# Optimization experiments

Hardware: AMD Instinct MI355X
Metric: run time of the kernel (lower is better)

Reference implementation:

```python
import jax, jax.numpy as jnp
import numpy as np

B, S, H = 1, 1024, 2048
NH, NKV, HD = 32, 4, 128
E, K, I = 32, 8, 768
EPS = 1e-06
ROPE_BASE = 1e6


def rmsnorm(x, w, eps=EPS):
    xf = x.astype(jnp.float32)
    var = jnp.mean(xf * xf, axis=-1, keepdims=True)
    return w * (xf * jax.lax.rsqrt(var + eps)).astype(x.dtype)


def apply_rope(x, cos, sin):
    # x: [B,S,N,HD]; cos/sin: [S,HD//2]; interleaved (llama-style) pair rotation
    xr = x.reshape(*x.shape[:-1], HD // 2, 2)
    x0, x1 = xr[..., 0], xr[..., 1]
    c = cos[None, :, None, :]
    s = sin[None, :, None, :]
    o0 = x0 * c - x1 * s
    o1 = x0 * s + x1 * c
    return jnp.stack([o0, o1], axis=-1).reshape(x.shape)


def setup_inputs() -> dict:
    key = jax.random.key(0)
    ks = jax.random.split(key, 16)
    hidden_states = jax.random.normal(ks[0], (B, S, H), dtype=jnp.float32)
    # RoPE angles: positions * inv_freq  -> [S, HD//2]
    inv_freq = 1.0 / (ROPE_BASE ** (np.arange(0, HD, 2, dtype=np.float32) / HD))
    position_embeddings = jnp.asarray(np.arange(S, dtype=np.float32)[:, None] * inv_freq[None, :])
    # causal additive mask [1,1,S,S]
    causal = jnp.tril(jnp.ones((S, S), dtype=bool))
    attention_mask = jnp.where(causal, 0.0, -1e9).astype(jnp.float32)[None, None]
    w = 0.02
    params = {
        'ln1_w': jnp.ones((H,), jnp.float32),
        'ln2_w': jnp.ones((H,), jnp.float32),
        'q_w': w * jax.random.normal(ks[1], (H, NH * HD), jnp.float32),
        'k_w': w * jax.random.normal(ks[2], (H, NKV * HD), jnp.float32),
        'v_w': w * jax.random.normal(ks[3], (H, NKV * HD), jnp.float32),
        'o_w': w * jax.random.normal(ks[4], (NH * HD, H), jnp.float32),
        'qn_w': jnp.ones((HD,), jnp.float32),
        'kn_w': jnp.ones((HD,), jnp.float32),
        'gate_w': w * jax.random.normal(ks[5], (H, E), jnp.float32),
        'wg': w * jax.random.normal(ks[6], (E, H, I), jnp.float32),
        'wu': w * jax.random.normal(ks[7], (E, H, I), jnp.float32),
        'wd': w * jax.random.normal(ks[8], (E, I, H), jnp.float32),
    }
    return {'hidden_states': hidden_states, 'position_embeddings': position_embeddings,
            'attention_mask': attention_mask, 'start_pos': 0, **params}


def reference(hidden_states, position_embeddings, attention_mask, start_pos,
              ln1_w, ln2_w, q_w, k_w, v_w, o_w, qn_w, kn_w, gate_w, wg, wu, wd):
    x = hidden_states  # [B,S,H]
    # --- attention ---
    h = rmsnorm(x, ln1_w)
    q = rmsnorm((h @ q_w).reshape(B, S, NH, HD), qn_w)
    k = rmsnorm((h @ k_w).reshape(B, S, NKV, HD), kn_w)
    v = (h @ v_w).reshape(B, S, NKV, HD)
    cos, sin = jnp.cos(position_embeddings), jnp.sin(position_embeddings)
    q = apply_rope(q, cos, sin)
    k = apply_rope(k, cos, sin)
    q = q.transpose(0, 2, 1, 3)  # [B,NH,S,HD]
    k = jnp.repeat(k.transpose(0, 2, 1, 3), NH // NKV, axis=1)
    v = jnp.repeat(v.transpose(0, 2, 1, 3), NH // NKV, axis=1)
    scores = jnp.einsum('bhqd,bhkd->bhqk', q, k) * (HD ** -0.5) + attention_mask
    attn = jax.nn.softmax(scores, axis=-1)
    o = jnp.einsum('bhqk,bhkd->bhqd', attn, v).transpose(0, 2, 1, 3).reshape(B, S, NH * HD)
    x = x + o @ o_w
    # --- MoE ---
    h = rmsnorm(x, ln2_w).reshape(B * S, H)  # [T,H]
    probs = jax.nn.softmax((h @ gate_w).astype(jnp.float32), axis=-1)
    rw, sel = jax.lax.top_k(probs, K)  # [T,K]
    rw = rw / jnp.sum(rw, axis=-1, keepdims=True)  # norm_topk_prob
    T = B * S
    # dense combine weights [T,E]; zero for unselected experts (same math as loop)
    wte = jnp.zeros((T, E), jnp.float32).at[jnp.arange(T)[:, None], sel].add(rw).astype(h.dtype)
    g = jnp.einsum('th,ehi->tei', h, wg)
    u = jnp.einsum('th,ehi->tei', h, wu)
    act = jax.nn.silu(g) * u  # [T,E,I]
    moe = jnp.einsum('te,tei,eih->th', wte, act, wd)
    return x + moe.reshape(B, S, H)
```

## Files before the change

kernel.cpp:

```cpp
#include <hip/hip_runtime.h>
#include <hip/hip_bf16.h>

#define S_ 1024
#define H_ 2048
#define NH_ 32
#define NKV_ 4
#define HD_ 128
#define NE_ 32
#define TOPK_ 8
#define I_ 768
#define EPS_ 1e-6f
#define QS_ 5120
#define BK2 32

typedef __bf16 bf16_t;
typedef __bf16 bf16x4v __attribute__((ext_vector_type(4)));
typedef __bf16 bf16x8 __attribute__((ext_vector_type(8)));
typedef float f32x4 __attribute__((ext_vector_type(4)));
typedef float f32x16 __attribute__((ext_vector_type(16)));
typedef unsigned short u16_t;
typedef unsigned int uint2v __attribute__((ext_vector_type(2)));
typedef unsigned int uint4v __attribute__((ext_vector_type(4)));

static __device__ __forceinline__ u16_t f2u(float x) {
  return __builtin_bit_cast(u16_t, (__bf16)x);
}
static __device__ __forceinline__ float u2f(u16_t u) {
  return (float)__builtin_bit_cast(__bf16, u);
}

static __device__ __forceinline__ void gload16(const bf16_t* g, bf16_t* l) {
  __builtin_amdgcn_global_load_lds(
      (const __attribute__((address_space(1))) unsigned int*)g,
      (__attribute__((address_space(3))) unsigned int*)l, 16, 0, 0);
}

static __device__ __forceinline__ int tile_lane_off(int lane) {
  return (lane >> 2) * 32 + (((lane & 3) ^ ((lane >> 3) & 3)) << 3);
}

template <bool WF32>
__global__ __launch_bounds__(256) void rmsnorm2_k(const float* __restrict__ x,
                                                  const float* __restrict__ w,
                                                  float* __restrict__ outf,
                                                  bf16_t* __restrict__ outb) {
  int r = blockIdx.x, tid = threadIdx.x;
  const float* xr = x + (size_t)r * H_;
  f32x4 a = *(const f32x4*)(xr + tid * 8);
  f32x4 b = *(const f32x4*)(xr + tid * 8 + 4);
  float ss = 0.f;
#pragma unroll
  for (int i = 0; i < 4; ++i) ss += a[i] * a[i] + b[i] * b[i];
#pragma unroll
  for (int m = 1; m < 64; m <<= 1) ss += __shfl_xor(ss, m);
  __shared__ float wsum[4];
  if ((tid & 63) == 0) wsum[tid >> 6] = ss;
  __syncthreads();
  ss = wsum[0] + wsum[1] + wsum[2] + wsum[3];
  float inv = rsqrtf(ss * (1.0f / H_) + EPS_);
  f32x4 w0 = *(const f32x4*)(w + tid * 8);
  f32x4 w1 = *(const f32x4*)(w + tid * 8 + 4);
  f32x4 o0, o1;
#pragma unroll
  for (int i = 0; i < 4; ++i) { o0[i] = a[i] * inv * w0[i]; o1[i] = b[i] * inv * w1[i]; }
  if constexpr (WF32) {
    *(f32x4*)(outf + (size_t)r * H_ + tid * 8) = o0;
    *(f32x4*)(outf + (size_t)r * H_ + tid * 8 + 4) = o1;
  }
  bf16x8 ob;
#pragma unroll
  for (int i = 0; i < 4; ++i) { ob[i] = (__bf16)o0[i]; ob[i + 4] = (__bf16)o1[i]; }
  *(bf16x8*)(outb + (size_t)r * H_ + tid * 8) = ob;
}

__global__ __launch_bounds__(256) void transp3_k(const float* __restrict__ in,
                                                 bf16_t* __restrict__ out, int R, int C) {
  __shared__ float tile[64][65];
  size_t z = (size_t)blockIdx.z * R * C;
  int tx = threadIdx.x & 15, ty = threadIdx.x >> 4;
  int r0 = blockIdx.y * 64, c0 = blockIdx.x * 64;
#pragma unroll
  for (int i = 0; i < 4; ++i) {
    f32x4 v = *(const f32x4*)(in + z + (size_t)(r0 + ty + i * 16) * C + c0 + tx * 4);
    tile[ty + i * 16][tx * 4 + 0] = v[0];
    tile[ty + i * 16][tx * 4 + 1] = v[1];
    tile[ty + i * 16][tx * 4 + 2] = v[2];
    tile[ty + i * 16][tx * 4 + 3] = v[3];
  }
  __syncthreads();
  int KT = R >> 5;
  int flat = threadIdx.x * 16;
  int lt = flat >> 9;
  int within = flat & 511;
  int nr = within >> 5;
  int kc = within & 31;
  int tn = lt >> 1, tk = lt & 1;
  bf16x8 o0, o1;
#pragma unroll
  for (int j = 0; j < 8; ++j) o0[j] = (bf16_t)tile[tk * 32 + kc + j][tn * 16 + nr];
#pragma unroll
  for (int j = 0; j < 8; ++j) o1[j] = (bf16_t)tile[tk * 32 + kc + 8 + j][tn * 16 + nr];
  size_t tidx = ((size_t)((c0 >> 4) + tn) * KT + (r0 >> 5) + tk) << 9;
  *(bf16x8*)(out + z + tidx + nr * 32 + kc) = o0;
  *(bf16x8*)(out + z + tidx + nr * 32 + kc + 8) = o1;
}

template <int BMT, int BNT, int WM, int WN, typename TC, bool RESID>
__global__ __launch_bounds__(512) void gemmd_k(
    const bf16_t* __restrict__ A, const bf16_t* __restrict__ Bt,
    const float* __restrict__ resid, TC* __restrict__ C, int M, int N, int K) {
  constexpr int MI = BMT / WM / 16;
  constexpr int NI = BNT / WN / 16;
  constexpr int ALW = BMT / 16 / 8;
  constexpr int NBL = BNT / 16;
  static_assert(NBL <= 8, "B wave loads");
  __shared__ __align__(16) bf16_t As[2][BMT][BK2];
  __shared__ __align__(16) bf16_t Bs[2][BNT][BK2];
  int tid = threadIdx.x, lane = tid & 63, w = tid >> 6;
  int m0 = blockIdx.x * BMT, n0 = blockIdx.y * BNT;
  int srow = lane >> 2;
  int schunk = ((lane & 3) ^ ((lane >> 3) & 3)) * 8;
  const bf16_t* asrc[ALW];
#pragma unroll
  for (int i = 0; i < ALW; ++i) {
    int r = (w * ALW + i) * 16 + srow;
    asrc[i] = A + (size_t)(m0 + r) * K + schunk;
  }
  bool hasB = (w < NBL);
  int brow = w * 16;
  const bf16_t* bsrc = nullptr;
  if (hasB)
    bsrc = Bt + ((size_t)((n0 + brow) >> 4) * (K >> 5)) * 512 + tile_lane_off(lane);

  int fr = lane & 15, g = lane >> 4;
  int rk = (g ^ ((fr >> 1) & 3)) * 8;
  int wm = w / WN, wn = w % WN;
  int rbase0 = wm * (BMT / WM), cbase0 = wn * (BNT / WN);
  f32x4 acc[MI][NI] = {};
  int NT = K / BK2;
  {
#pragma unroll
    for (int i = 0; i < ALW; ++i) gload16(asrc[i], &As[0][(w * ALW + i) * 16][0]);
    if (hasB) gload16(bsrc, &Bs[0][brow][0]);
  }
  __syncthreads();
  int cur = 0;
  for (int t = 0; t < NT; ++t) {
    if (t + 1 < NT) {
      int ko = (t + 1) * BK2;
#pragma unroll
      for (int i = 0; i < ALW; ++i) gload16(asrc[i] + ko, &As[cur ^ 1][(w * ALW + i) * 16][0]);
      if (hasB) gload16(bsrc + (size_t)(t + 1) * 512, &Bs[cur ^ 1][brow][0]);
    }
    bf16x8 af[MI], bf[NI];
#pragma unroll
    for (int i = 0; i < MI; ++i) af[i] = *(const bf16x8*)&As[cur][rbase0 + i * 16 + fr][rk];
#pragma unroll
    for (int i = 0; i < NI; ++i) bf[i] = *(const bf16x8*)&Bs[cur][cbase0 + i * 16 + fr][rk];
#pragma unroll
    for (int mi = 0; mi < MI; ++mi)
#pragma unroll
      for (int ni = 0; ni < NI; ++ni)
        acc[mi][ni] = __builtin_amdgcn_mfma_f32_16x16x32_bf16(af[mi], bf[ni], acc[mi][ni], 0, 0, 0);
    __syncthreads();
    cur ^= 1;
  }
  int rbase = g * 4;
#pragma unroll
  for (int mi = 0; mi < MI; ++mi)
#pragma unroll
    for (int ni = 0; ni < NI; ++ni)
#pragma unroll
      for (int r = 0; r < 4; ++r) {
        int gi = m0 + rbase0 + mi * 16 + rbase + r;
        int gc = n0 + cbase0 + ni * 16 + fr;
        float v = acc[mi][ni][r];
        if constexpr (RESID) v += resid[(size_t)gi * N + gc];
        C[(size_t)gi * N + gc] = (TC)v;
      }
}

template <int BNT, int WM, int WN, typename TC, bool GATHER, bool SCALE, bool DUAL>
__global__ __launch_bounds__(512) void gemme2_k(
    const bf16_t* __restrict__ A, const bf16_t* __restrict__ B1g,
    const bf16_t* __restrict__ B2g, TC* __restrict__ C, bf16_t* __restrict__ act,
    const float* __restrict__ wlist, const int* __restrict__ counts,
    const int* __restrict__ offsets, const int* __restrict__ toklist,
    const int* __restrict__ mslots, const int* __restrict__ meta,
    int* __restrict__ qhead, int NTN, int N, int K) {
  constexpr int BMT = 128;
  constexpr int MI = BMT / WM / 16;
  constexpr int NI = BNT / WN / 16;
  constexpr int BNTT = BNT * (DUAL ? 2 : 1);
  constexpr int NBT = BNTT / 16;
  constexpr int BPW = NBT / 8;
  static_assert(BPW * 8 == NBT, "B tile split");
  __shared__ __align__(16) bf16_t As[4][BMT][BK2];
  __shared__ __align__(16) bf16_t Bs[4][BNTT][BK2];
  __shared__ int s_w;
  int tid = threadIdx.x, lane = tid & 63, w = tid >> 6;
  int srow = lane >> 2;
  int schunk = ((lane & 3) ^ ((lane >> 3) & 3)) * 8;
  int tloff = tile_lane_off(lane);
  int fr = lane & 15, g = lane >> 4;
  int rk = (g ^ ((fr >> 1) & 3)) * 8;
  int wm = w / WN, wn = w % WN;
  int rbase0 = wm * (BMT / WM), cbase0 = wn * (BNT / WN);
  int KT = K >> 5;
  int SS = K >> 7;
  int total = meta[0] * NTN;
  for (;;) {
    if (tid == 0) s_w = atomicAdd(qhead, 1);
    __syncthreads();
    int wk = s_w;
    if (wk >= total) return;
    int ms = mslots[wk / NTN];
    int n0 = (wk % NTN) * BNT;
    int e = ms >> 8, m0 = (ms & 255) * BMT;
    int cnt = counts[e], off = offsets[e];
    size_t bs = (size_t)K * N;
    const bf16_t* B1 = B1g + (size_t)e * bs;
    const bf16_t* B2 = DUAL ? (B2g + (size_t)e * bs) : nullptr;
    const bf16_t* asrc;
    {
      int gr = min(m0 + w * 16 + srow, cnt - 1);
      size_t grow;
      if constexpr (GATHER) grow = (size_t)toklist[e * S_ + gr];
      else grow = (size_t)(off + gr);
      asrc = A + grow * (size_t)K + schunk;
    }
    const bf16_t* bsrc[BPW];
    int brow16[BPW];
#pragma unroll
    for (int j = 0; j < BPW; ++j) {
      int r16 = (w * BPW + j) * 16;
      brow16[j] = r16;
      const bf16_t* Bb = (r16 < BNT) ? B1 : B2;
      int rr = (r16 < BNT) ? r16 : r16 - BNT;
      bsrc[j] = Bb + ((size_t)((n0 + rr) >> 4) * KT) * 512 + tloff;
    }
    f32x4 acc1[MI][NI] = {};
    f32x4 acc2[DUAL ? MI : 1][DUAL ? NI : 1] = {};
    for (int ss = 0; ss < SS; ++ss) {
      int kbase = ss * 128;
#pragma unroll
      for (int sub = 0; sub < 4; ++sub)
        gload16(asrc + kbase + sub * BK2, &As[sub][w * 16][0]);
#pragma unroll
      for (int j = 0; j < BPW; ++j)
#pragma unroll
        for (int sub = 0; sub < 4; ++sub)
          gload16(bsrc[j] + (size_t)(ss * 4 + sub) * 512, &Bs[sub][brow16[j]][0]);
      __syncthreads();
#pragma unroll
      for (int sub = 0; sub < 4; ++sub) {
        bf16x8 af[MI], b1f[NI], b2f[DUAL ? NI : 1];
#pragma unroll
        for (int i = 0; i < MI; ++i) af[i] = *(const bf16x8*)&As[sub][rbase0 + i * 16 + fr][rk];
#pragma unroll
        for (int i = 0; i < NI; ++i) b1f[i] = *(const bf16x8*)&Bs[sub][cbase0 + i * 16 + fr][rk];
        if constexpr (DUAL) {
#pragma unroll
          for (int i = 0; i < NI; ++i) b2f[i] = *(const bf16x8*)&Bs[sub][BNT + cbase0 + i * 16 + fr][rk];
        }
#pragma unroll
        for (int mi = 0; mi < MI; ++mi)
#pragma unroll
          for (int ni = 0; ni < NI; ++ni) {
            acc1[mi][ni] = __builtin_amdgcn_mfma_f32_16x16x32_bf16(af[mi], b1f[ni], acc1[mi][ni], 0, 0, 0);
            if constexpr (DUAL)
              acc2[mi][ni] = __builtin_amdgcn_mfma_f32_16x16x32_bf16(af[mi], b2f[ni], acc2[mi][ni], 0, 0, 0);
          }
      }
      __syncthreads();
    }
    int rbase = g * 4;
#pragma unroll
    for (int mi = 0; mi < MI; ++mi)
#pragma unroll
      for (int ni = 0; ni < NI; ++ni)
#pragma unroll
        for (int r = 0; r < 4; ++r) {
          int lr = rbase0 + mi * 16 + rbase + r;
          int gi = m0 + lr;
          if (gi >= cnt) continue;
          int gc = n0 + cbase0 + ni * 16 + fr;
          if constexpr (DUAL) {
            float gv = acc1[mi][ni][r], uv = acc2[mi][ni][r];
            float sig = 1.0f / (1.0f + __expf(-gv));
            act[(size_t)(off + gi) * N + gc] = (bf16_t)(gv * sig * uv);
          } else {
            float v = acc1[mi][ni][r];
            if constexpr (SCALE) v *= wlist[(size_t)e * S_ + gi];
            C[(size_t)(off + gi) * N + gc] = (TC)v;
          }
        }
  }
}

__global__ __launch_bounds__(64) void qkpack_k(const float* __restrict__ qkv,
                                               const float* __restrict__ qn,
                                               const float* __restrict__ kn,
                                               const float* __restrict__ pe,
                                               bf16_t* __restrict__ Q2,
                                               bf16_t* __restrict__ K2) {
  int s = blockIdx.x, hh = blockIdx.y, lane = threadIdx.x;
  const float* ptr;
  const float* w;
  if (hh < NH_) { ptr = qkv + (size_t)s * QS_ + hh * HD_; w = qn; }
  else          { ptr = qkv + (size_t)s * QS_ + NH_ * HD_ + (hh - NH_) * HD_; w = kn; }
  float x0 = ptr[2 * lane], x1 = ptr[2 * lane + 1];
  float ss = x0 * x0 + x1 * x1;
#pragma unroll
  for (int m = 1; m < 64; m <<= 1) ss += __shfl_xor(ss, m);
  float inv = rsqrtf(ss * (1.0f / HD_) + EPS_);
  x0 = x0 * inv * w[2 * lane];
  x1 = x1 * inv * w[2 * lane + 1];
  float ang = pe[(size_t)s * (HD_ / 2) + lane];
  float sn, cs;
  sincosf(ang, &sn, &cs);
  float r0 = x0 * cs - x1 * sn;
  float r1 = x0 * sn + x1 * cs;
  if (hh < NH_) {
    const float scale = 0.08838834764831845f;
    float a = r0 * scale, b = r1 * scale;
    u16_t h0 = f2u(a), h1 = f2u(b);
    unsigned hw = (unsigned)h0 | ((unsigned)h1 << 16);
    unsigned lw = (unsigned)f2u(a - u2f(h0)) | ((unsigned)f2u(b - u2f(h1)) << 16);
    unsigned* base = (unsigned*)(Q2 + ((size_t)s * NH_ + hh) * 256);
    base[lane] = hw;
    base[64 + lane] = lw;
  } else {
    u16_t h0 = f2u(r0), h1 = f2u(r1);
    unsigned hw = (unsigned)h0 | ((unsigned)h1 << 16);
    unsigned lw = (unsigned)f2u(r0 - u2f(h0)) | ((unsigned)f2u(r1 - u2f(h1)) << 16);
    int j = lane >> 2, off = (2 * lane) & 7;
    unsigned* base = (unsigned*)(K2 + ((size_t)(hh - NH_) * S_ + s) * 256);
    base[(((j) ^ (s & 31)) * 8 + off) >> 1] = hw;
    base[(((16 + j) ^ (s & 31)) * 8 + off) >> 1] = lw;
  }
}

__global__ __launch_bounds__(256) void vpack_k(const float* __restrict__ qkv,
                                               bf16_t* __restrict__ V2T) {
  int t = blockIdx.x, kvh = blockIdx.y;
  int kv0 = t * 64;
  bf16_t* dst = V2T + (size_t)(kvh * 16 + t) * 128 * 128;
  const float* vbase = qkv + NH_ * HD_ + NKV_ * HD_ + kvh * HD_;
#pragma unroll
  for (int i = 0; i < 4; ++i) {
    int flat = threadIdx.x + i * 256;
    int kvp = flat >> 5, d4 = (flat & 31) * 4;
    const float* r0 = vbase + (size_t)(kv0 + 2 * kvp) * QS_ + d4;
    const float* r1 = r0 + QS_;
    f32x4 a = *(const f32x4*)r0;
    f32x4 b = *(const f32x4*)r1;
    int kvg = (2 * kvp) >> 3, sub = (2 * kvp) & 7;
#pragma unroll
    for (int e = 0; e < 4; ++e) {
      int d = d4 + e;
      int fsw = (d ^ (d >> 4)) & 15;
      u16_t ha = f2u(a[e]), hb = f2u(b[e]);
      unsigned hw = (unsigned)ha | ((unsigned)hb << 16);
      unsigned lw = (unsigned)f2u(a[e] - u2f(ha)) | ((unsigned)f2u(b[e] - u2f(hb)) << 16);
      unsigned* dd = (unsigned*)(dst + d * 128);
      dd[((kvg ^ fsw) * 8 + sub) >> 1] = hw;
      dd[(((8 + kvg) ^ fsw) * 8 + sub) >> 1] = lw;
    }
  }
}

#define AKV 64
__global__ __launch_bounds__(512, 2) void attn6_k(const bf16_t* __restrict__ Q2,
                                                  const bf16_t* __restrict__ K2,
                                                  const bf16_t* __restrict__ V2T,
                                                  bf16_t* __restrict__ o) {
  int q0 = blockIdx.x * 32;
  int kvh = blockIdx.y;
  int tid = threadIdx.x, lane = tid & 63, w = tid >> 6;
  int g = lane >> 5, c32 = lane & 31;
  int h = kvh * 8 + w;
  int qrow = q0 + c32;
  int last_t = (q0 + 31) >> 6;
  __shared__ __align__(16) u16_t Kl[AKV * 256];
  __shared__ __align__(16) u16_t Vl[128 * 128];

  bf16x8 qh[8], ql[8];
  {
    const bf16_t* qp2 = Q2 + ((size_t)qrow * NH_ + h) * 256;
#pragma unroll
    for (int ks = 0; ks < 8; ++ks) {
      qh[ks] = *(const bf16x8*)(qp2 + g * 8 + ks * 16);
      ql[ks] = *(const bf16x8*)(qp2 + 128 + g * 8 + ks * 16);
    }
  }

  f32x16 accO[4] = {};
  float m = -3.0e38f, l = 0.f;

  for (int t = 0; t <= last_t; ++t) {
    int kv0 = t * AKV;
    __syncthreads();
    {
      const bf16_t* ksrc = K2 + ((size_t)kvh * S_ + kv0) * 256;
#pragma unroll
      for (int i = 0; i < 4; ++i) {
        int cbase = w * 64 + i * 512;
        gload16(ksrc + (size_t)(cbase + lane) * 8, (bf16_t*)&Kl[cbase * 8]);
      }
    }
    {
      const bf16_t* vsrc = V2T + (size_t)(kvh * 16 + t) * 128 * 128;
#pragma unroll
      for (int i = 0; i < 4; ++i) {
        int cbase = w * 64 + i * 512;
        gload16(vsrc + (size_t)(cbase + lane) * 8, (bf16_t*)&Vl[cbase * 8]);
      }
    }
    __syncthreads();

    f32x16 accS[2] = {};
#pragma unroll
    for (int ks = 0; ks < 8; ++ks) {
      int db = g * 8 + ks * 16;
#pragma unroll
      for (int mf = 0; mf < 2; ++mf) {
        int kvr = c32 + mf * 32;
        bf16x8 ah = *(const bf16x8*)&Kl[kvr * 256 + (((db >> 3)) ^ c32) * 8];
        bf16x8 al = *(const bf16x8*)&Kl[kvr * 256 + ((16 + (db >> 3)) ^ c32) * 8];
        accS[mf] = __builtin_amdgcn_mfma_f32_32x32x16_bf16(ah, qh[ks], accS[mf], 0, 0, 0);
        accS[mf] = __builtin_amdgcn_mfma_f32_32x32x16_bf16(ah, ql[ks], accS[mf], 0, 0, 0);
        accS[mf] = __builtin_amdgcn_mfma_f32_32x32x16_bf16(al, qh[ks], accS[mf], 0, 0, 0);
      }
    }
    float p[2][16];
    float tmax = -3.0e38f;
#pragma unroll
    for (int mf = 0; mf < 2; ++mf)
#pragma unroll
      for (int r = 0; r < 16; ++r) {
        int kvg = kv0 + mf * 32 + (r & 3) + 8 * (r >> 2) + 4 * g;
        float s = (kvg <= qrow) ? accS[mf][r] : -3.0e38f;
        p[mf][r] = s;
        tmax = fmaxf(tmax, s);
      }
    tmax = fmaxf(tmax, __shfl_xor(tmax, 32));
    float mn = fmaxf(m, tmax);
    float sc = __expf(m - mn);
    float ts = 0.f;
#pragma unroll
    for (int mf = 0; mf < 2; ++mf)
#pragma unroll
      for (int r = 0; r < 16; ++r) {
        float e = __expf(p[mf][r] - mn);
        p[mf][r] = e;
        ts += e;
      }
    ts += __shfl_xor(ts, 32);
    l = l * sc + ts;
    m = mn;
#pragma unroll
    for (int r = 0; r < 16; ++r) {
      int row16 = (r & 3) + 8 * (r >> 2) + 4 * g;
      float scr = __shfl(sc, row16);
#pragma unroll
      for (int nf = 0; nf < 4; ++nf) accO[nf][r] *= scr;
    }
#pragma unroll
    for (int ks = 0; ks < 4; ++ks) {
      int k1 = ks & 1, mf = ks >> 1;
      unsigned Lh[4], Ll[4];
#pragma unroll
      for (int i = 0; i < 4; ++i) {
        float a = p[mf][8 * k1 + 2 * i], b = p[mf][8 * k1 + 2 * i + 1];
        u16_t ha = f2u(a), hb = f2u(b);
        Lh[i] = (unsigned)ha | ((unsigned)hb << 16);
        Ll[i] = (unsigned)f2u(a - u2f(ha)) | ((unsigned)f2u(b - u2f(hb)) << 16);
      }
      unsigned Xh[4], Xl[4];
#pragma unroll
      for (int i = 0; i < 4; ++i) {
        Xh[i] = (unsigned)__shfl_xor((int)Lh[i], 32);
        Xl[i] = (unsigned)__shfl_xor((int)Ll[i], 32);
      }
      uint4v fh, fl;
      fh[0] = g ? Xh[2] : Lh[0]; fh[1] = g ? Xh[3] : Lh[1];
      fh[2] = g ? Lh[2] : Xh[0]; fh[3] = g ? Lh[3] : Xh[1];
      fl[0] = g ? Xl[2] : Ll[0]; fl[1] = g ? Xl[3] : Ll[1];
      fl[2] = g ? Ll[2] : Xl[0]; fl[3] = g ? Ll[3] : Xl[1];
      bf16x8 pH = __builtin_bit_cast(bf16x8, fh);
      bf16x8 pL = __builtin_bit_cast(bf16x8, fl);
      int kvb = g * 8 + ks * 16;
#pragma unroll
      for (int nf = 0; nf < 4; ++nf) {
        int d = c32 + nf * 32;
        int fsw = (d ^ (d >> 4)) & 15;
        bf16x8 vh = *(const bf16x8*)&Vl[d * 128 + (((kvb >> 3)) ^ fsw) * 8];
        bf16x8 vl = *(const bf16x8*)&Vl[d * 128 + ((8 + (kvb >> 3)) ^ fsw) * 8];
        accO[nf] = __builtin_amdgcn_mfma_f32_32x32x16_bf16(pH, vh, accO[nf], 0, 0, 0);
        accO[nf] = __builtin_amdgcn_mfma_f32_32x32x16_bf16(pH, vl, accO[nf], 0, 0, 0);
        accO[nf] = __builtin_amdgcn_mfma_f32_32x32x16_bf16(pL, vh, accO[nf], 0, 0, 0);
      }
    }
  }
  float invl = 1.0f / l;
#pragma unroll
  for (int r = 0; r < 16; ++r) {
    int row16 = (r & 3) + 8 * (r >> 2) + 4 * g;
    float il = __shfl(invl, row16);
    int orow = q0 + row16;
#pragma unroll
    for (int nf = 0; nf < 4; ++nf)
      o[((size_t)orow * NH_ + h) * HD_ + nf * 32 + c32] = (bf16_t)(accO[nf][r] * il);
  }
}

__global__ __launch_bounds__(256) void router2_k(const float* __restrict__ h2,
                                                 const float* __restrict__ gw,
                                                 int* __restrict__ sel,
                                                 float* __restrict__ wsel) {
  int t = blockIdx.x, tid = threadIdx.x;
  int e = tid & 31, grp = tid >> 5;
  float acc = 0.f;
  for (int kk = grp; kk < H_; kk += 8)
    acc += h2[(size_t)t * H_ + kk] * gw[(size_t)kk * NE_ + e];
  __shared__ float part[8][32];
  part[grp][e] = acc;
  __syncthreads();
  if (tid < 64) {
    int lane = tid;
    float lg = -3.0e38f;
    if (lane < 32) {
      lg = 0.f;
      for (int g = 0; g < 8; ++g) lg += part[g][lane];
    }
    float tm = lg;
#pragma unroll
    for (int mm = 1; mm < 32; mm <<= 1) tm = fmaxf(tm, __shfl_xor(tm, mm));
    if (lane < 32) lg = __expf(lg - tm);
    bool avail = (lane < 32);
    float tot = 0.f;
    int se[TOPK_]; float rw[TOPK_];
#pragma unroll
    for (int kk = 0; kk < TOPK_; ++kk) {
      float val = avail ? lg : -1.f;
      float best = val;
#pragma unroll
      for (int mm = 1; mm < 32; mm <<= 1) best = fmaxf(best, __shfl_xor(best, mm));
      unsigned long long ball = __ballot(avail && (val == best));
      int bi = (int)__builtin_ctzll(ball);
      if (lane == bi) avail = false;
      se[kk] = bi;
      rw[kk] = best;
      tot += best;
    }
    float itot = 1.0f / tot;
    if (lane == 0) {
#pragma unroll
      for (int kk = 0; kk < TOPK_; ++kk) {
        sel[t * TOPK_ + kk] = se[kk];
        wsel[t * TOPK_ + kk] = rw[kk] * itot;
      }
    }
  }
}

__global__ __launch_bounds__(64) void build_k(const int* __restrict__ sel,
                                              const float* __restrict__ wsel,
                                              int* __restrict__ counts,
                                              int* __restrict__ toklist,
                                              float* __restrict__ wlist,
                                              int* __restrict__ pos) {
  int e = blockIdx.x, lane = threadIdx.x;
  int base = 0;
  for (int c = 0; c < S_ / 64; ++c) {
    int t = c * 64 + lane;
    int match = -1;
#pragma unroll
    for (int k = 0; k < TOPK_; ++k)
      if (sel[t * TOPK_ + k] == e) match = k;
    bool flag = (match >= 0);
    unsigned long long mask = __ballot(flag);
    int prefix = __popcll(mask & ((1ull << lane) - 1ull));
    if (flag) {
      int p = base + prefix;
      toklist[e * S_ + p] = t;
      wlist[e * S_ + p] = wsel[t * TOPK_ + match];
      pos[t * TOPK_ + match] = p;
    }
    base += __popcll(mask);
  }
  if (lane == 0) counts[e] = base;
}

__global__ void scan_k(const int* __restrict__ counts, int* __restrict__ offsets,
                       int* __restrict__ mslots, int* __restrict__ meta,
                       int* __restrict__ qheads) {
  if (threadIdx.x == 0 && blockIdx.x == 0) {
    int o = 0, ns = 0;
    for (int e = 0; e < NE_; ++e) {
      offsets[e] = o;
      int c = counts[e];
      for (int m0 = 0; m0 < c; m0 += 128) mslots[ns++] = (e << 8) | (m0 >> 7);
      o += c;
    }
    offsets[NE_] = o;
    meta[0] = ns;
    qheads[0] = 0;
    qheads[1] = 0;
  }
}

__global__ __launch_bounds__(256) void combine_k(const float* __restrict__ x1,
                                                 const bf16_t* __restrict__ pairout,
                                                 const int* __restrict__ sel,
                                                 const int* __restrict__ pos,
                                                 const int* __restrict__ offsets,
                                                 float* __restrict__ out) {
  int t = blockIdx.x, tid = threadIdx.x;
  int slots[TOPK_];
#pragma unroll
  for (int kk = 0; kk < TOPK_; ++kk)
    slots[kk] = offsets[sel[t * TOPK_ + kk]] + pos[t * TOPK_ + kk];
  int c = tid * 8;
  f32x4 s0 = *(const f32x4*)(x1 + (size_t)t * H_ + c);
  f32x4 s1 = *(const f32x4*)(x1 + (size_t)t * H_ + c + 4);
#pragma unroll
  for (int kk = 0; kk < TOPK_; ++kk) {
    bf16x8 pv = *(const bf16x8*)(pairout + (size_t)slots[kk] * H_ + c);
#pragma unroll
    for (int i = 0; i < 4; ++i) { s0[i] += (float)pv[i]; s1[i] += (float)pv[i + 4]; }
  }
  *(f32x4*)(out + (size_t)t * H_ + c) = s0;
  *(f32x4*)(out + (size_t)t * H_ + c + 4) = s1;
}

extern "C" void kernel_launch(void* const* d_in, const int* in_sizes, int n_in,
                              void* d_out, int out_size, void* d_ws, size_t ws_size,
                              hipStream_t stream) {
  const float* hidden = (const float*)d_in[0];
  const float* pe     = (const float*)d_in[1];
  const float* ln1    = (const float*)d_in[4];
  const float* ln2    = (const float*)d_in[5];
  const float* q_w    = (const float*)d_in[6];
  const float* k_w    = (const float*)d_in[7];
  const float* v_w    = (const float*)d_in[8];
  const float* o_w    = (const float*)d_in[9];
  const float* qn     = (const float*)d_in[10];
  const float* kn     = (const float*)d_in[11];
  const float* gate_w = (const float*)d_in[12];
  const float* wg     = (const float*)d_in[13];
  const float* wu     = (const float*)d_in[14];
  const float* wd     = (const float*)d_in[15];
  float* out = (float*)d_out;

  char* p = (char*)d_ws;
  auto alloc = [&](size_t bytes) {
    char* r = p;
    p += (bytes + 255) & ~(size_t)255;
    return r;
  };
  bf16_t* h1b     = (bf16_t*)alloc((size_t)S_ * H_ * 2);
  float*  qkv     = (float*)alloc((size_t)S_ * QS_ * 4);
  bf16_t* Q2      = (bf16_t*)alloc((size_t)S_ * NH_ * 256 * 2);
  bf16_t* K2      = (bf16_t*)alloc((size_t)NKV_ * S_ * 256 * 2);
  bf16_t* V2T     = (bf16_t*)alloc((size_t)NKV_ * 16 * 128 * 128 * 2);
  bf16_t* aob     = (bf16_t*)alloc((size_t)S_ * NH_ * HD_ * 2);
  float*  x1      = (float*)alloc((size_t)S_ * H_ * 4);
  float*  h2      = (float*)alloc((size_t)S_ * H_ * 4);
  bf16_t* h2b     = (bf16_t*)alloc((size_t)S_ * H_ * 2);
  bf16_t* act     = (bf16_t*)alloc((size_t)S_ * TOPK_ * I_ * 2);
  bf16_t* po      = (bf16_t*)alloc((size_t)S_ * TOPK_ * H_ * 2);
  int*    counts  = (int*)alloc(NE_ * 4);
  int*    offs    = (int*)alloc((NE_ + 1) * 4);
  int*    toklist = (int*)alloc((size_t)NE_ * S_ * 4);
  float*  wlist   = (float*)alloc((size_t)NE_ * S_ * 4);
  int*    sel     = (int*)alloc((size_t)S_ * TOPK_ * 4);
  float*  wsel    = (float*)alloc((size_t)S_ * TOPK_ * 4);
  int*    pos     = (int*)alloc((size_t)S_ * TOPK_ * 4);
  int*    mslots  = (int*)alloc(512 * 4);
  int*    meta    = (int*)alloc(4);
  int*    qheads  = (int*)alloc(2 * 4);
  bf16_t* qkvT = (bf16_t*)alloc((size_t)QS_ * H_ * 2);
  bf16_t* owT  = (bf16_t*)alloc((size_t)(NH_ * HD_) * H_ * 2);
  bf16_t* wgT  = (bf16_t*)alloc((size_t)NE_ * H_ * I_ * 2);
  bf16_t* wuT  = (bf16_t*)alloc((size_t)NE_ * H_ * I_ * 2);
  bf16_t* wdT  = (bf16_t*)alloc((size_t)NE_ * I_ * H_ * 2);
  bf16_t* qwTp = qkvT;
  bf16_t* kwTp = qkvT + (size_t)(NH_ * HD_) * H_;
  bf16_t* vwTp = qkvT + (size_t)(NH_ * HD_ + NKV_ * HD_) * H_;

  transp3_k<<<dim3((NH_ * HD_) / 64, H_ / 64, 1), 256, 0, stream>>>(q_w, qwTp, H_, NH_ * HD_);
  transp3_k<<<dim3((NKV_ * HD_) / 64, H_ / 64, 1), 256, 0, stream>>>(k_w, kwTp, H_, NKV_ * HD_);
  transp3_k<<<dim3((NKV_ * HD_) / 64, H_ / 64, 1), 256, 0, stream>>>(v_w, vwTp, H_, NKV_ * HD_);
  transp3_k<<<dim3(H_ / 64, (NH_ * HD_) / 64, 1), 256, 0, stream>>>(o_w, owT, NH_ * HD_, H_);
  transp3_k<<<dim3(I_ / 64, H_ / 64, NE_), 256, 0, stream>>>(wg, wgT, H_, I_);
  transp3_k<<<dim3(I_ / 64, H_ / 64, NE_), 256, 0, stream>>>(wu, wuT, H_, I_);
  transp3_k<<<dim3(H_ / 64, I_ / 64, NE_), 256, 0, stream>>>(wd, wdT, I_, H_);

  rmsnorm2_k<false><<<S_, 256, 0, stream>>>(hidden, ln1, nullptr, h1b);
  gemmd_k<256, 128, 4, 2, float, false>
      <<<dim3(S_ / 256, QS_ / 128), 512, 0, stream>>>(h1b, qkvT, nullptr, qkv, S_, QS_, H_);
  qkpack_k<<<dim3(S_, NH_ + NKV_), 64, 0, stream>>>(qkv, qn, kn, pe, Q2, K2);
  vpack_k<<<dim3(16, NKV_), 256, 0, stream>>>(qkv, V2T);
  attn6_k<<<dim3(S_ / 32, NKV_), 512, 0, stream>>>(Q2, K2, V2T, aob);
  gemmd_k<128, 64, 4, 2, float, true>
      <<<dim3(S_ / 128, H_ / 64), 512, 0, stream>>>(aob, owT, hidden, x1, S_, H_, NH_ * HD_);
  rmsnorm2_k<true><<<S_, 256, 0, stream>>>(x1, ln2, h2, h2b);
  router2_k<<<S_, 256, 0, stream>>>(h2, gate_w, sel, wsel);
  build_k<<<NE_, 64, 0, stream>>>(sel, wsel, counts, toklist, wlist, pos);
  scan_k<<<1, 64, 0, stream>>>(counts, offs, mslots, meta, qheads);
  gemme2_k<128, 2, 4, float, true, false, true>
      <<<256, 512, 0, stream>>>(h2b, wgT, wuT, nullptr, act, wlist, counts, offs, toklist,
                                mslots, meta, &qheads[0], I_ / 128, I_, H_);
  gemme2_k<256, 2, 4, bf16_t, false, true, false>
      <<<256, 512, 0, stream>>>(act, wdT, nullptr, po, nullptr, wlist, counts, offs, nullptr,
                                mslots, meta, &qheads[1], H_ / 256, H_, I_);
  combine_k<<<S_, 256, 0, stream>>>(x1, po, sel, pos, offs, out);
}
```

Measured before the change: 782.5 us.

## Load MoE expert weight fragments directly to registers and use taller token tiles

```diff
diff --git a/kernel.cpp b/kernel.cpp
--- a/kernel.cpp
+++ b/kernel.cpp
@@ -180,30 +180,26 @@
       }
 }
 
-template <int BNT, int WM, int WN, typename TC, bool GATHER, bool SCALE, bool DUAL>
-__global__ __launch_bounds__(512) void gemme2_k(
+template <int BNT, typename TC, bool GATHER, bool SCALE, bool DUAL>
+__global__ __launch_bounds__(512) void gemme3_k(
     const bf16_t* __restrict__ A, const bf16_t* __restrict__ B1g,
     const bf16_t* __restrict__ B2g, TC* __restrict__ C, bf16_t* __restrict__ act,
     const float* __restrict__ wlist, const int* __restrict__ counts,
     const int* __restrict__ offsets, const int* __restrict__ toklist,
     const int* __restrict__ mslots, const int* __restrict__ meta,
     int* __restrict__ qhead, int NTN, int N, int K) {
-  constexpr int BMT = 128;
+  constexpr int BMT = 256;
+  constexpr int WM = 4, WN = 2;
   constexpr int MI = BMT / WM / 16;
   constexpr int NI = BNT / WN / 16;
-  constexpr int BNTT = BNT * (DUAL ? 2 : 1);
-  constexpr int NBT = BNTT / 16;
-  constexpr int BPW = NBT / 8;
-  static_assert(BPW * 8 == NBT, "B tile split");
   __shared__ __align__(16) bf16_t As[4][BMT][BK2];
-  __shared__ __align__(16) bf16_t Bs[4][BNTT][BK2];
   __shared__ int s_w;
   int tid = threadIdx.x, lane = tid & 63, w = tid >> 6;
   int srow = lane >> 2;
   int schunk = ((lane & 3) ^ ((lane >> 3) & 3)) * 8;
-  int tloff = tile_lane_off(lane);
   int fr = lane & 15, g = lane >> 4;
   int rk = (g ^ ((fr >> 1) & 3)) * 8;
+  int froff = fr * 32 + g * 8;
   int wm = w / WN, wn = w % WN;
   int rbase0 = wm * (BMT / WM), cbase0 = wn * (BNT / WN);
   int KT = K >> 5;
@@ -221,55 +217,55 @@
     size_t bs = (size_t)K * N;
     const bf16_t* B1 = B1g + (size_t)e * bs;
     const bf16_t* B2 = DUAL ? (B2g + (size_t)e * bs) : nullptr;
-    const bf16_t* asrc;
-    {
-      int gr = min(m0 + w * 16 + srow, cnt - 1);
+    const bf16_t* asrc[2];
+#pragma unroll
+    for (int i = 0; i < 2; ++i) {
+      int gr = min(m0 + (w * 2 + i) * 16 + srow, cnt - 1);
       size_t grow;
       if constexpr (GATHER) grow = (size_t)toklist[e * S_ + gr];
       else grow = (size_t)(off + gr);
-      asrc = A + grow * (size_t)K + schunk;
-    }
-    const bf16_t* bsrc[BPW];
-    int brow16[BPW];
-#pragma unroll
-    for (int j = 0; j < BPW; ++j) {
-      int r16 = (w * BPW + j) * 16;
-      brow16[j] = r16;
-      const bf16_t* Bb = (r16 < BNT) ? B1 : B2;
-      int rr = (r16 < BNT) ? r16 : r16 - BNT;
-      bsrc[j] = Bb + ((size_t)((n0 + rr) >> 4) * KT) * 512 + tloff;
+      asrc[i] = A + grow * (size_t)K + schunk;
+    }
+    const bf16_t* b1base[NI];
+    const bf16_t* b2base[DUAL ? NI : 1];
+#pragma unroll
+    for (int i = 0; i < NI; ++i) {
+      size_t tn = (size_t)((n0 + cbase0 + i * 16) >> 4);
+      b1base[i] = B1 + tn * KT * 512 + froff;
+      if constexpr (DUAL) b2base[i] = B2 + tn * KT * 512 + froff;
     }
     f32x4 acc1[MI][NI] = {};
     f32x4 acc2[DUAL ? MI : 1][DUAL ? NI : 1] = {};
     for (int ss = 0; ss < SS; ++ss) {
       int kbase = ss * 128;
 #pragma unroll
+      for (int i = 0; i < 2; ++i)
+#pragma unroll
+        for (int sub = 0; sub < 4; ++sub)
+          gload16(asrc[i] + kbase + sub * BK2, &As[sub][(w * 2 + i) * 16][0]);
+      bf16x8 b1f[4][NI];
+      bf16x8 b2f[DUAL ? 4 : 1][DUAL ? NI : 1];
+#pragma unroll
       for (int sub = 0; sub < 4; ++sub)
-        gload16(asrc + kbase + sub * BK2, &As[sub][w * 16][0]);
-#pragma unroll
-      for (int j = 0; j < BPW; ++j)
-#pragma unroll
-        for (int sub = 0; sub < 4; ++sub)
-          gload16(bsrc[j] + (size_t)(ss * 4 + sub) * 512, &Bs[sub][brow16[j]][0]);
+#pragma unroll
+        for (int i = 0; i < NI; ++i) {
+          b1f[sub][i] = *(const bf16x8*)(b1base[i] + (size_t)(ss * 4 + sub) * 512);
+          if constexpr (DUAL)
+            b2f[sub][i] = *(const bf16x8*)(b2base[i] + (size_t)(ss * 4 + sub) * 512);
+        }
       __syncthreads();
 #pragma unroll
       for (int sub = 0; sub < 4; ++sub) {
-        bf16x8 af[MI], b1f[NI], b2f[DUAL ? NI : 1];
+        bf16x8 af[MI];
 #pragma unroll
         for (int i = 0; i < MI; ++i) af[i] = *(const bf16x8*)&As[sub][rbase0 + i * 16 + fr][rk];
 #pragma unroll
-        for (int i = 0; i < NI; ++i) b1f[i] = *(const bf16x8*)&Bs[sub][cbase0 + i * 16 + fr][rk];
-        if constexpr (DUAL) {
-#pragma unroll
-          for (int i = 0; i < NI; ++i) b2f[i] = *(const bf16x8*)&Bs[sub][BNT + cbase0 + i * 16 + fr][rk];
-        }
-#pragma unroll
         for (int mi = 0; mi < MI; ++mi)
 #pragma unroll
           for (int ni = 0; ni < NI; ++ni) {
-            acc1[mi][ni] = __builtin_amdgcn_mfma_f32_16x16x32_bf16(af[mi], b1f[ni], acc1[mi][ni], 0, 0, 0);
+            acc1[mi][ni] = __builtin_amdgcn_mfma_f32_16x16x32_bf16(af[mi], b1f[sub][ni], acc1[mi][ni], 0, 0, 0);
             if constexpr (DUAL)
-              acc2[mi][ni] = __builtin_amdgcn_mfma_f32_16x16x32_bf16(af[mi], b2f[ni], acc2[mi][ni], 0, 0, 0);
+              acc2[mi][ni] = __builtin_amdgcn_mfma_f32_16x16x32_bf16(af[mi], b2f[sub][ni], acc2[mi][ni], 0, 0, 0);
           }
       }
       __syncthreads();
@@ -601,7 +597,7 @@
     for (int e = 0; e < NE_; ++e) {
       offsets[e] = o;
       int c = counts[e];
-      for (int m0 = 0; m0 < c; m0 += 128) mslots[ns++] = (e << 8) | (m0 >> 7);
+      for (int m0 = 0; m0 < c; m0 += 256) mslots[ns++] = (e << 8) | (m0 >> 8);
       o += c;
     }
     offsets[NE_] = o;
@@ -710,11 +706,11 @@
   router2_k<<<S_, 256, 0, stream>>>(h2, gate_w, sel, wsel);
   build_k<<<NE_, 64, 0, stream>>>(sel, wsel, counts, toklist, wlist, pos);
   scan_k<<<1, 64, 0, stream>>>(counts, offs, mslots, meta, qheads);
-  gemme2_k<128, 2, 4, float, true, false, true>
-      <<<256, 512, 0, stream>>>(h2b, wgT, wuT, nullptr, act, wlist, counts, offs, toklist,
-                                mslots, meta, &qheads[0], I_ / 128, I_, H_);
-  gemme2_k<256, 2, 4, bf16_t, false, true, false>
-      <<<256, 512, 0, stream>>>(act, wdT, nullptr, po, nullptr, wlist, counts, offs, nullptr,
-                                mslots, meta, &qheads[1], H_ / 256, H_, I_);
+  gemme3_k<64, float, true, false, true>
+      <<<512, 512, 0, stream>>>(h2b, wgT, wuT, nullptr, act, wlist, counts, offs, toklist,
+                                mslots, meta, &qheads[0], I_ / 64, I_, H_);
+  gemme3_k<128, bf16_t, false, true, false>
+      <<<512, 512, 0, stream>>>(act, wdT, nullptr, po, nullptr, wlist, counts, offs, nullptr,
+                                mslots, meta, &qheads[1], H_ / 128, H_, I_);
   combine_k<<<S_, 256, 0, stream>>>(x1, po, sel, pos, offs, out);
 }
```

After: 901.3 us. +15.2%, slower.
